# Kernel tuning notes

Measured on AMD Instinct MI355X. Metric: run time of the kernel, lower is better.

The kernel has to match this reference:

```python
import jax, jax.numpy as jnp
import numpy as np

N_NODES = 50000
N_EDGES = 800000
IN_CH = 128
HID = 64   # 2 * out_channels
OUT = 32   # out_channels
SLOPE = 0.2  # PyG GATConv default negative_slope


def _gat_layer(x, W, a_src, a_dst, b, src, dst):
    """Single-head GATConv: proj -> edge attention logits -> segment softmax
    over destination nodes -> scatter-aggregate weighted source messages."""
    n = x.shape[0]
    h = x @ W                                   # [N, C]
    ls = h @ a_src                              # [N] per-node src score
    ld = h @ a_dst                              # [N] per-node dst score
    logits = jax.nn.leaky_relu(ls[src] + ld[dst], negative_slope=SLOPE)  # [E]
    # numerically stable segment softmax grouped by destination node
    lmax = jax.ops.segment_max(logits, dst, num_segments=n)              # [N]
    e = jnp.exp(logits - lmax[dst])                                      # [E]
    denom = jax.ops.segment_sum(e, dst, num_segments=n)                  # [N]
    alpha = e / denom[dst]                                               # [E]
    out = jax.ops.segment_sum(alpha[:, None] * h[src], dst, num_segments=n)
    return out + b


def setup_inputs() -> dict:
    key = jax.random.key(0)
    ks = jax.random.split(key, 10)
    x = jax.random.normal(ks[0], (N_NODES, IN_CH), dtype=jnp.float32)
    edge_index = jax.random.randint(ks[1], (2, N_EDGES), 0, N_NODES, dtype=jnp.int32)
    s1 = 1.0 / np.sqrt(IN_CH)
    s2 = 1.0 / np.sqrt(HID)
    return {
        "x": x,
        "edge_index": edge_index,
        "W1": jax.random.normal(ks[2], (IN_CH, HID), dtype=jnp.float32) * s1,
        "a_src1": jax.random.normal(ks[3], (HID,), dtype=jnp.float32) * s2,
        "a_dst1": jax.random.normal(ks[4], (HID,), dtype=jnp.float32) * s2,
        "b1": jnp.zeros((HID,), dtype=jnp.float32),
        "W2": jax.random.normal(ks[5], (HID, OUT), dtype=jnp.float32) * s2,
        "a_src2": jax.random.normal(ks[6], (OUT,), dtype=jnp.float32) / np.sqrt(OUT),
        "a_dst2": jax.random.normal(ks[7], (OUT,), dtype=jnp.float32) / np.sqrt(OUT),
        "b2": jnp.zeros((OUT,), dtype=jnp.float32),
    }


def reference(x, edge_index, W1, a_src1, a_dst1, b1, W2, a_src2, a_dst2, b2):
    src, dst = edge_index[0], edge_index[1]
    h = jax.nn.relu(_gat_layer(x, W1, a_src1, a_dst1, b1, src, dst))
    return _gat_layer(h, W2, a_src2, a_dst2, b2, src, dst)
```

## Files before the change

kernel.cpp:

```cpp
#include <hip/hip_runtime.h>


#define N_NODES 50000
#define N_EDGES 800000
#define SLOPE 0.2f
#define NBUCK 196
#define CAP 4608

__global__ __launch_bounds__(256) void k_zerobins(int* __restrict__ binctr)
{
    if (threadIdx.x < NBUCK) binctr[threadIdx.x] = 0;
}

__global__ __launch_bounds__(1024) void k_bin(
    const int* __restrict__ src, const int* __restrict__ dst,
    int* __restrict__ binctr,
    int* __restrict__ stg_src, int* __restrict__ stg_dst)
{
    __shared__ int hist[NBUCK];
    __shared__ int gb[NBUCK];
    const int t = threadIdx.x;
    if (t < NBUCK) hist[t] = 0;
    __syncthreads();

    const int base = blockIdx.x * 8192;
    int ms[8], md[8], mr[8];
    int n = 0;
    #pragma unroll
    for (int k = 0; k < 8; ++k) {
        int e = base + t + k * 1024;
        if (e < N_EDGES) {
            int s = src[e], d = dst[e];
            ms[n] = s; md[n] = d;
            mr[n] = atomicAdd(&hist[d >> 8], 1);
            ++n;
        }
    }
    __syncthreads();
    if (t < NBUCK) gb[t] = atomicAdd(&binctr[t], hist[t]);
    __syncthreads();
    for (int i = 0; i < n; ++i) {
        int b = md[i] >> 8;
        int p = b * CAP + gb[b] + mr[i];
        stg_src[p] = ms[i];
        stg_dst[p] = md[i];
    }
}

__global__ __launch_bounds__(256) void k_btot(
    const int* __restrict__ binctr, int* __restrict__ bucket_base)
{
    __shared__ int tmp[256];
    const int t = threadIdx.x;
    int v = (t < NBUCK) ? binctr[t] : 0;
    tmp[t] = v;
    __syncthreads();
    #pragma unroll
    for (int off = 1; off < 256; off <<= 1) {
        int u = (t >= off) ? tmp[t - off] : 0;
        __syncthreads();
        tmp[t] += u;
        __syncthreads();
    }
    if (t < NBUCK) bucket_base[t] = tmp[t] - v;
}

__global__ __launch_bounds__(1024) void k_sort(
    const int* __restrict__ stg_src, const int* __restrict__ stg_dst,
    const int* __restrict__ binctr, const int* __restrict__ bucket_base,
    int* __restrict__ row_start, int* __restrict__ csr_src)
{
    __shared__ int cnt[256];
    __shared__ int off[256];
    const int b = blockIdx.x, t = threadIdx.x;
    const int n = binctr[b];
    const int sbase = b * CAP;
    const int obase = bucket_base[b];

    if (t < 256) cnt[t] = 0;
    __syncthreads();

    int ms[5], mk[5], mr[5];
    int c = 0;
    for (int i = t; i < n; i += 1024) {
        int s = stg_src[sbase + i], d = stg_dst[sbase + i];
        int k = d & 255;
        ms[c] = s; mk[c] = k;
        mr[c] = atomicAdd(&cnt[k], 1);
        ++c;
    }
    __syncthreads();

    if (t < 256) off[t] = cnt[t];
    __syncthreads();
    #pragma unroll
    for (int o = 1; o < 256; o <<= 1) {
        int u = (t < 256 && t >= o) ? off[t - o] : 0;
        __syncthreads();
        if (t < 256) off[t] += u;
        __syncthreads();
    }

    if (t < 256) {
        int node = b * 256 + t;
        if (node < N_NODES) row_start[node] = obase + off[t] - cnt[t];
    }
    if (b == NBUCK - 1 && t == 0) row_start[N_NODES] = N_EDGES;

    for (int i = 0; i < c; ++i)
        csr_src[obase + off[mk[i]] - cnt[mk[i]] + mr[i]] = ms[i];
}

__global__ __launch_bounds__(256) void k_gemm1(
    const float* __restrict__ x, const float* __restrict__ W1,
    const float* __restrict__ a_src, const float* __restrict__ a_dst,
    float* __restrict__ h1, float* __restrict__ ls, float* __restrict__ ld)
{
    __shared__ float As[64][128];
    __shared__ float Bs[128][64];
    const int tid = threadIdx.x;
    const int m0 = blockIdx.x * 64;

    {
        const float4* Wv = (const float4*)W1;
        float4* Bv = (float4*)&Bs[0][0];
        #pragma unroll
        for (int i = 0; i < 8; ++i) Bv[tid + i * 256] = Wv[tid + i * 256];
    }
    {
        const float4* Xv = (const float4*)x;
        #pragma unroll
        for (int i = 0; i < 8; ++i) {
            int idx = tid + i * 256;
            int r = idx >> 5, kq = idx & 31;
            float4 v = make_float4(0.f, 0.f, 0.f, 0.f);
            if (m0 + r < N_NODES) v = Xv[(size_t)(m0 + r) * 32 + kq];
            ((float4*)&As[r][0])[kq] = v;
        }
    }
    __syncthreads();

    const int tx = tid & 15, ty = tid >> 4;
    const int c0 = tx * 4, r0 = ty * 4;
    float acc[4][4] = {};
    for (int k = 0; k < 128; k += 4) {
        float a_s[4][4];
        #pragma unroll
        for (int i = 0; i < 4; ++i) {
            float4 av = *(const float4*)&As[r0 + i][k];
            a_s[i][0] = av.x; a_s[i][1] = av.y; a_s[i][2] = av.z; a_s[i][3] = av.w;
        }
        #pragma unroll
        for (int kk = 0; kk < 4; ++kk) {
            float4 b = *(const float4*)&Bs[k + kk][c0];
            #pragma unroll
            for (int i = 0; i < 4; ++i) {
                acc[i][0] += a_s[i][kk] * b.x;
                acc[i][1] += a_s[i][kk] * b.y;
                acc[i][2] += a_s[i][kk] * b.z;
                acc[i][3] += a_s[i][kk] * b.w;
            }
        }
    }

    float as4[4], ad4[4];
    #pragma unroll
    for (int j = 0; j < 4; ++j) { as4[j] = a_src[c0 + j]; ad4[j] = a_dst[c0 + j]; }

    #pragma unroll
    for (int i = 0; i < 4; ++i) {
        int row = m0 + r0 + i;
        float pls = acc[i][0]*as4[0] + acc[i][1]*as4[1] + acc[i][2]*as4[2] + acc[i][3]*as4[3];
        float pld = acc[i][0]*ad4[0] + acc[i][1]*ad4[1] + acc[i][2]*ad4[2] + acc[i][3]*ad4[3];
        #pragma unroll
        for (int off = 1; off < 16; off <<= 1) {
            pls += __shfl_xor(pls, off, 64);
            pld += __shfl_xor(pld, off, 64);
        }
        if (row < N_NODES) {
            ((float4*)&h1[(size_t)row * 64])[tx] =
                make_float4(acc[i][0], acc[i][1], acc[i][2], acc[i][3]);
            if (tx == 0) { ls[row] = pls; ld[row] = pld; }
        }
    }
}

__global__ __launch_bounds__(256) void k_agg1(
    const int* __restrict__ csr_src, const int* __restrict__ row_start,
    const float* __restrict__ ls, const float* __restrict__ ld,
    const float* __restrict__ h1, const float* __restrict__ b1,
    float* __restrict__ acc1)
{
    const int node = blockIdx.x * 4 + (threadIdx.x >> 6);
    const int lane = threadIdx.x & 63;
    const int beg = row_start[node], end = row_start[node + 1];
    const float ldv = ld[node];

    float acc = 0.f, sw = 0.f;
    for (int base = beg; base < end; base += 64) {
        const int cnt = min(64, end - base);
        int s = 0;
        float w = 0.f;
        if (lane < cnt) {
            s = csr_src[base + lane];
            float l = ls[s] + ldv;
            l = l > 0.f ? l : SLOPE * l;
            w = __expf(l);
        }
        float wsum = w;
        #pragma unroll
        for (int off = 1; off < 64; off <<= 1) wsum += __shfl_xor(wsum, off, 64);
        sw += wsum;

        int j = 0;
        for (; j + 4 <= cnt; j += 4) {
            int s0 = __shfl(s, j, 64),     s1 = __shfl(s, j + 1, 64);
            int s2 = __shfl(s, j + 2, 64), s3 = __shfl(s, j + 3, 64);
            float w0 = __shfl(w, j, 64),     w1 = __shfl(w, j + 1, 64);
            float w2 = __shfl(w, j + 2, 64), w3 = __shfl(w, j + 3, 64);
            float g0 = h1[(size_t)s0 * 64 + lane];
            float g1 = h1[(size_t)s1 * 64 + lane];
            float g2 = h1[(size_t)s2 * 64 + lane];
            float g3 = h1[(size_t)s3 * 64 + lane];
            acc += w0 * g0; acc += w1 * g1; acc += w2 * g2; acc += w3 * g3;
        }
        for (; j < cnt; ++j) {
            int sj = __shfl(s, j, 64);
            float wj = __shfl(w, j, 64);
            acc += wj * h1[(size_t)sj * 64 + lane];
        }
    }
    float r = sw > 0.f ? acc / sw : 0.f;
    acc1[(size_t)node * 64 + lane] = r + b1[lane];
}

__global__ __launch_bounds__(256) void k_epi1(
    const float* __restrict__ acc1, const float* __restrict__ W2,
    const float* __restrict__ a_src2, const float* __restrict__ a_dst2,
    float* __restrict__ h2, float* __restrict__ ls2, float* __restrict__ ld2)
{
    __shared__ float Hs[64][68];
    __shared__ float W2s[64][32];
    const int tid = threadIdx.x;
    const int n0 = blockIdx.x * 64;

    {
        const float4* Wv = (const float4*)W2;
        float4* Ws = (float4*)&W2s[0][0];
        Ws[tid] = Wv[tid];
        Ws[tid + 256] = Wv[tid + 256];
    }
    {
        const float4* Av = (const float4*)acc1;
        #pragma unroll
        for (int i = 0; i < 4; ++i) {
            int idx = tid + i * 256;
            int r = idx >> 4, kq = idx & 15;
            float4 v = make_float4(0.f, 0.f, 0.f, 0.f);
            if (n0 + r < N_NODES) {
                v = Av[(size_t)(n0 + r) * 16 + kq];
                v.x = fmaxf(v.x, 0.f); v.y = fmaxf(v.y, 0.f);
                v.z = fmaxf(v.z, 0.f); v.w = fmaxf(v.w, 0.f);
            }
            ((float4*)&Hs[r][0])[kq] = v;
        }
    }
    __syncthreads();

    const int nl = tid >> 2, cg = tid & 3, c0 = cg * 8;
    float acc[8] = {};
    for (int k4 = 0; k4 < 16; ++k4) {
        float4 hv4 = *(const float4*)&Hs[nl][k4 * 4];
        #pragma unroll
        for (int kk = 0; kk < 4; ++kk) {
            float hv = kk == 0 ? hv4.x : kk == 1 ? hv4.y : kk == 2 ? hv4.z : hv4.w;
            int k = k4 * 4 + kk;
            float4 w0 = *(const float4*)&W2s[k][c0];
            float4 w1 = *(const float4*)&W2s[k][c0 + 4];
            acc[0] += hv * w0.x; acc[1] += hv * w0.y;
            acc[2] += hv * w0.z; acc[3] += hv * w0.w;
            acc[4] += hv * w1.x; acc[5] += hv * w1.y;
            acc[6] += hv * w1.z; acc[7] += hv * w1.w;
        }
    }

    float pls = 0.f, pld = 0.f;
    #pragma unroll
    for (int j = 0; j < 8; ++j) {
        pls += acc[j] * a_src2[c0 + j];
        pld += acc[j] * a_dst2[c0 + j];
    }
    pls += __shfl_xor(pls, 1, 64); pls += __shfl_xor(pls, 2, 64);
    pld += __shfl_xor(pld, 1, 64); pld += __shfl_xor(pld, 2, 64);

    int node = n0 + nl;
    if (node < N_NODES) {
        ((float4*)&h2[(size_t)node * 32])[cg * 2] =
            make_float4(acc[0], acc[1], acc[2], acc[3]);
        ((float4*)&h2[(size_t)node * 32])[cg * 2 + 1] =
            make_float4(acc[4], acc[5], acc[6], acc[7]);
        if (cg == 0) { ls2[node] = pls; ld2[node] = pld; }
    }
}

__global__ __launch_bounds__(256) void k_agg2(
    const int* __restrict__ csr_src, const int* __restrict__ row_start,
    const float* __restrict__ ls, const float* __restrict__ ld,
    const float* __restrict__ h2, const float* __restrict__ b2,
    float* __restrict__ out)
{
    const int idx = blockIdx.x * 256 + threadIdx.x;
    const int node = idx >> 5;
    const int c = idx & 31;
    const int beg = row_start[node], end = row_start[node + 1];
    const float ldv = ld[node];

    float acc = 0.f, sw = 0.f;
    for (int base = beg; base < end; base += 32) {
        const int cnt = min(32, end - base);
        int s = 0;
        float w = 0.f;
        if (c < cnt) {
            s = csr_src[base + c];
            float l = ls[s] + ldv;
            l = l > 0.f ? l : SLOPE * l;
            w = __expf(l);
        }
        float wsum = w;
        #pragma unroll
        for (int off = 1; off < 32; off <<= 1) wsum += __shfl_xor(wsum, off, 32);
        sw += wsum;

        int j = 0;
        for (; j + 4 <= cnt; j += 4) {
            int s0 = __shfl(s, j, 32),     s1 = __shfl(s, j + 1, 32);
            int s2 = __shfl(s, j + 2, 32), s3 = __shfl(s, j + 3, 32);
            float w0 = __shfl(w, j, 32),     w1 = __shfl(w, j + 1, 32);
            float w2 = __shfl(w, j + 2, 32), w3 = __shfl(w, j + 3, 32);
            float g0 = h2[(size_t)s0 * 32 + c];
            float g1 = h2[(size_t)s1 * 32 + c];
            float g2 = h2[(size_t)s2 * 32 + c];
            float g3 = h2[(size_t)s3 * 32 + c];
            acc += w0 * g0; acc += w1 * g1; acc += w2 * g2; acc += w3 * g3;
        }
        for (; j < cnt; ++j) {
            int sj = __shfl(s, j, 32);
            float wj = __shfl(w, j, 32);
            acc += wj * h2[(size_t)sj * 32 + c];
        }
    }
    float r = sw > 0.f ? acc / sw : 0.f;
    out[(size_t)node * 32 + c] = r + b2[c];
}

extern "C" void kernel_launch(void* const* d_in, const int* in_sizes, int n_in,
                              void* d_out, int out_size, void* d_ws, size_t ws_size,
                              hipStream_t stream)
{
    const float* x      = (const float*)d_in[0];
    const int*   ei     = (const int*)  d_in[1];
    const float* W1     = (const float*)d_in[2];
    const float* a_src1 = (const float*)d_in[3];
    const float* a_dst1 = (const float*)d_in[4];
    const float* b1     = (const float*)d_in[5];
    const float* W2     = (const float*)d_in[6];
    const float* a_src2 = (const float*)d_in[7];
    const float* a_dst2 = (const float*)d_in[8];
    const float* b2     = (const float*)d_in[9];
    const int* src = ei;
    const int* dst = ei + N_EDGES;
    float* out = (float*)d_out;

    float* ws   = (float*)d_ws;
    float* h1   = ws;
    float* acc1 = ws + 3200000;
    float* ls1  = ws + 6400000;
    float* ld1  = ws + 6450000;
    int* row_start   = (int*)(ws + 6500000);
    int* csr_src     = (int*)(ws + 6550016);
    int* binctr      = (int*)(ws + 7350016);
    int* bucket_base = (int*)(ws + 7350272);
    int* stg_src = (int*)h1;
    int* stg_dst = (int*)acc1;
    float* h2  = h1;
    float* ls2 = ls1;
    float* ld2 = ld1;

    k_zerobins<<<1,   256,  0, stream>>>(binctr);
    k_bin     <<<98,  1024, 0, stream>>>(src, dst, binctr, stg_src, stg_dst);
    k_btot    <<<1,   256,  0, stream>>>(binctr, bucket_base);
    k_sort    <<<NBUCK, 1024, 0, stream>>>(stg_src, stg_dst, binctr, bucket_base,
                                           row_start, csr_src);

    k_gemm1<<<782,   256, 0, stream>>>(x, W1, a_src1, a_dst1, h1, ls1, ld1);
    k_agg1 <<<12500, 256, 0, stream>>>(csr_src, row_start, ls1, ld1, h1, b1, acc1);

    k_epi1 <<<782,  256, 0, stream>>>(acc1, W2, a_src2, a_dst2, h2, ls2, ld2);
    k_agg2 <<<6250, 256, 0, stream>>>(csr_src, row_start, ls2, ld2, h2, b2, out);
}
```

Measured before the change: 201.7 us.

## Pack staging edges into one word and vectorize aggregation gathers with float4

The binning stage now packs the source index and the low 8 bits of the destination into a single 32-bit word, so the staging traffic is halved and a single array is read in the sort pass. Both aggregation kernels now have each lane gather a float4 of a source row, with several edges processed in parallel across lane groups and then reduced through cross-lane shuffles. This aims to cut the number of gather instructions and improve memory-level parallelism on the irregular h-row loads. The cost is extra shuffle reductions at the end and only a fraction of lanes writing the output. Packing relies on node ids fitting in 16 bits, which holds for 50000 nodes.

```diff
diff --git a/kernel.cpp b/kernel.cpp
--- a/kernel.cpp
+++ b/kernel.cpp
@@ -14,8 +14,7 @@
 
 __global__ __launch_bounds__(1024) void k_bin(
     const int* __restrict__ src, const int* __restrict__ dst,
-    int* __restrict__ binctr,
-    int* __restrict__ stg_src, int* __restrict__ stg_dst)
+    int* __restrict__ binctr, int* __restrict__ stg)
 {
     __shared__ int hist[NBUCK];
     __shared__ int gb[NBUCK];
@@ -24,27 +23,25 @@
     __syncthreads();
 
     const int base = blockIdx.x * 8192;
-    int ms[8], md[8], mr[8];
+    int mp[8], mb[8], mr[8];
     int n = 0;
     #pragma unroll
     for (int k = 0; k < 8; ++k) {
         int e = base + t + k * 1024;
         if (e < N_EDGES) {
             int s = src[e], d = dst[e];
-            ms[n] = s; md[n] = d;
-            mr[n] = atomicAdd(&hist[d >> 8], 1);
+            int b = d >> 8;
+            mp[n] = s | ((d & 255) << 16);
+            mb[n] = b;
+            mr[n] = atomicAdd(&hist[b], 1);
             ++n;
         }
     }
     __syncthreads();
     if (t < NBUCK) gb[t] = atomicAdd(&binctr[t], hist[t]);
     __syncthreads();
-    for (int i = 0; i < n; ++i) {
-        int b = md[i] >> 8;
-        int p = b * CAP + gb[b] + mr[i];
-        stg_src[p] = ms[i];
-        stg_dst[p] = md[i];
-    }
+    for (int i = 0; i < n; ++i)
+        stg[mb[i] * CAP + gb[mb[i]] + mr[i]] = mp[i];
 }
 
 __global__ __launch_bounds__(256) void k_btot(
@@ -66,7 +63,7 @@
 }
 
 __global__ __launch_bounds__(1024) void k_sort(
-    const int* __restrict__ stg_src, const int* __restrict__ stg_dst,
+    const int* __restrict__ stg,
     const int* __restrict__ binctr, const int* __restrict__ bucket_base,
     int* __restrict__ row_start, int* __restrict__ csr_src)
 {
@@ -80,12 +77,13 @@
     if (t < 256) cnt[t] = 0;
     __syncthreads();
 
-    int ms[5], mk[5], mr[5];
+    int mv[5], mk[5], mr[5];
     int c = 0;
     for (int i = t; i < n; i += 1024) {
-        int s = stg_src[sbase + i], d = stg_dst[sbase + i];
-        int k = d & 255;
-        ms[c] = s; mk[c] = k;
+        int v = stg[sbase + i];
+        int k = v >> 16;
+        mv[c] = v & 0xFFFF;
+        mk[c] = k;
         mr[c] = atomicAdd(&cnt[k], 1);
         ++c;
     }
@@ -108,7 +106,7 @@
     if (b == NBUCK - 1 && t == 0) row_start[N_NODES] = N_EDGES;
 
     for (int i = 0; i < c; ++i)
-        csr_src[obase + off[mk[i]] - cnt[mk[i]] + mr[i]] = ms[i];
+        csr_src[obase + off[mk[i]] - cnt[mk[i]] + mr[i]] = mv[i];
 }
 
 __global__ __launch_bounds__(256) void k_gemm1(
@@ -193,10 +191,13 @@
 {
     const int node = blockIdx.x * 4 + (threadIdx.x >> 6);
     const int lane = threadIdx.x & 63;
+    const int c4 = lane & 15, eslot = lane >> 4;
     const int beg = row_start[node], end = row_start[node + 1];
     const float ldv = ld[node];
-
-    float acc = 0.f, sw = 0.f;
+    const float4* H = (const float4*)h1;
+
+    float4 acc = make_float4(0.f, 0.f, 0.f, 0.f);
+    float sw = 0.f;
     for (int base = beg; base < end; base += 64) {
         const int cnt = min(64, end - base);
         int s = 0;
@@ -213,25 +214,40 @@
         sw += wsum;
 
         int j = 0;
-        for (; j + 4 <= cnt; j += 4) {
-            int s0 = __shfl(s, j, 64),     s1 = __shfl(s, j + 1, 64);
-            int s2 = __shfl(s, j + 2, 64), s3 = __shfl(s, j + 3, 64);
-            float w0 = __shfl(w, j, 64),     w1 = __shfl(w, j + 1, 64);
-            float w2 = __shfl(w, j + 2, 64), w3 = __shfl(w, j + 3, 64);
-            float g0 = h1[(size_t)s0 * 64 + lane];
-            float g1 = h1[(size_t)s1 * 64 + lane];
-            float g2 = h1[(size_t)s2 * 64 + lane];
-            float g3 = h1[(size_t)s3 * 64 + lane];
-            acc += w0 * g0; acc += w1 * g1; acc += w2 * g2; acc += w3 * g3;
-        }
-        for (; j < cnt; ++j) {
-            int sj = __shfl(s, j, 64);
-            float wj = __shfl(w, j, 64);
-            acc += wj * h1[(size_t)sj * 64 + lane];
-        }
-    }
-    float r = sw > 0.f ? acc / sw : 0.f;
-    acc1[(size_t)node * 64 + lane] = r + b1[lane];
+        for (; j + 8 <= cnt; j += 8) {
+            int   s0 = __shfl(s, j + eslot, 64);
+            int   s1 = __shfl(s, j + 4 + eslot, 64);
+            float w0 = __shfl(w, j + eslot, 64);
+            float w1 = __shfl(w, j + 4 + eslot, 64);
+            float4 g0 = H[(size_t)s0 * 16 + c4];
+            float4 g1 = H[(size_t)s1 * 16 + c4];
+            acc.x += w0 * g0.x; acc.y += w0 * g0.y;
+            acc.z += w0 * g0.z; acc.w += w0 * g0.w;
+            acc.x += w1 * g1.x; acc.y += w1 * g1.y;
+            acc.z += w1 * g1.z; acc.w += w1 * g1.w;
+        }
+        for (; j < cnt; j += 4) {
+            int   sj = __shfl(s, j + eslot, 64);
+            float wj = __shfl(w, j + eslot, 64);
+            float4 g = H[(size_t)sj * 16 + c4];
+            acc.x += wj * g.x; acc.y += wj * g.y;
+            acc.z += wj * g.z; acc.w += wj * g.w;
+        }
+    }
+    #pragma unroll
+    for (int off = 16; off < 64; off <<= 1) {
+        acc.x += __shfl_xor(acc.x, off, 64);
+        acc.y += __shfl_xor(acc.y, off, 64);
+        acc.z += __shfl_xor(acc.z, off, 64);
+        acc.w += __shfl_xor(acc.w, off, 64);
+    }
+    if (eslot == 0) {
+        float inv = sw > 0.f ? 1.f / sw : 0.f;
+        float4 bb = ((const float4*)b1)[c4];
+        ((float4*)&acc1[(size_t)node * 64])[c4] =
+            make_float4(acc.x * inv + bb.x, acc.y * inv + bb.y,
+                        acc.z * inv + bb.z, acc.w * inv + bb.w);
+    }
 }
 
 __global__ __launch_bounds__(256) void k_epi1(
@@ -311,17 +327,20 @@
 {
     const int idx = blockIdx.x * 256 + threadIdx.x;
     const int node = idx >> 5;
-    const int c = idx & 31;
+    const int grp = idx & 31;
+    const int c4 = grp & 7, eslot = grp >> 3;
     const int beg = row_start[node], end = row_start[node + 1];
     const float ldv = ld[node];
-
-    float acc = 0.f, sw = 0.f;
+    const float4* H = (const float4*)h2;
+
+    float4 acc = make_float4(0.f, 0.f, 0.f, 0.f);
+    float sw = 0.f;
     for (int base = beg; base < end; base += 32) {
         const int cnt = min(32, end - base);
         int s = 0;
         float w = 0.f;
-        if (c < cnt) {
-            s = csr_src[base + c];
+        if (grp < cnt) {
+            s = csr_src[base + grp];
             float l = ls[s] + ldv;
             l = l > 0.f ? l : SLOPE * l;
             w = __expf(l);
@@ -332,25 +351,40 @@
         sw += wsum;
 
         int j = 0;
-        for (; j + 4 <= cnt; j += 4) {
-            int s0 = __shfl(s, j, 32),     s1 = __shfl(s, j + 1, 32);
-            int s2 = __shfl(s, j + 2, 32), s3 = __shfl(s, j + 3, 32);
-            float w0 = __shfl(w, j, 32),     w1 = __shfl(w, j + 1, 32);
-            float w2 = __shfl(w, j + 2, 32), w3 = __shfl(w, j + 3, 32);
-            float g0 = h2[(size_t)s0 * 32 + c];
-            float g1 = h2[(size_t)s1 * 32 + c];
-            float g2 = h2[(size_t)s2 * 32 + c];
-            float g3 = h2[(size_t)s3 * 32 + c];
-            acc += w0 * g0; acc += w1 * g1; acc += w2 * g2; acc += w3 * g3;
-        }
-        for (; j < cnt; ++j) {
-            int sj = __shfl(s, j, 32);
-            float wj = __shfl(w, j, 32);
-            acc += wj * h2[(size_t)sj * 32 + c];
-        }
-    }
-    float r = sw > 0.f ? acc / sw : 0.f;
-    out[(size_t)node * 32 + c] = r + b2[c];
+        for (; j + 8 <= cnt; j += 8) {
+            int   s0 = __shfl(s, j + eslot, 32);
+            int   s1 = __shfl(s, j + 4 + eslot, 32);
+            float w0 = __shfl(w, j + eslot, 32);
+            float w1 = __shfl(w, j + 4 + eslot, 32);
+            float4 g0 = H[(size_t)s0 * 8 + c4];
+            float4 g1 = H[(size_t)s1 * 8 + c4];
+            acc.x += w0 * g0.x; acc.y += w0 * g0.y;
+            acc.z += w0 * g0.z; acc.w += w0 * g0.w;
+            acc.x += w1 * g1.x; acc.y += w1 * g1.y;
+            acc.z += w1 * g1.z; acc.w += w1 * g1.w;
+        }
+        for (; j < cnt; j += 4) {
+            int   sj = __shfl(s, j + eslot, 32);
+            float wj = __shfl(w, j + eslot, 32);
+            float4 g = H[(size_t)sj * 8 + c4];
+            acc.x += wj * g.x; acc.y += wj * g.y;
+            acc.z += wj * g.z; acc.w += wj * g.w;
+        }
+    }
+    #pragma unroll
+    for (int off = 8; off < 32; off <<= 1) {
+        acc.x += __shfl_xor(acc.x, off, 32);
+        acc.y += __shfl_xor(acc.y, off, 32);
+        acc.z += __shfl_xor(acc.z, off, 32);
+        acc.w += __shfl_xor(acc.w, off, 32);
+    }
+    if (eslot == 0) {
+        float inv = sw > 0.f ? 1.f / sw : 0.f;
+        float4 bb = ((const float4*)b2)[c4];
+        ((float4*)&out[(size_t)node * 32])[c4] =
+            make_float4(acc.x * inv + bb.x, acc.y * inv + bb.y,
+                        acc.z * inv + bb.z, acc.w * inv + bb.w);
+    }
 }
 
 extern "C" void kernel_launch(void* const* d_in, const int* in_sizes, int n_in,
@@ -380,16 +414,15 @@
     int* csr_src     = (int*)(ws + 6550016);
     int* binctr      = (int*)(ws + 7350016);
     int* bucket_base = (int*)(ws + 7350272);
-    int* stg_src = (int*)h1;
-    int* stg_dst = (int*)acc1;
+    int* stg = (int*)h1;
     float* h2  = h1;
     float* ls2 = ls1;
     float* ld2 = ld1;
 
     k_zerobins<<<1,   256,  0, stream>>>(binctr);
-    k_bin     <<<98,  1024, 0, stream>>>(src, dst, binctr, stg_src, stg_dst);
+    k_bin     <<<98,  1024, 0, stream>>>(src, dst, binctr, stg);
     k_btot    <<<1,   256,  0, stream>>>(binctr, bucket_base);
-    k_sort    <<<NBUCK, 1024, 0, stream>>>(stg_src, stg_dst, binctr, bucket_base,
+    k_sort    <<<NBUCK, 1024, 0, stream>>>(stg, binctr, bucket_base,
                                            row_start, csr_src);
 
     k_gemm1<<<782,   256, 0, stream>>>(x, W1, a_src1, a_dst1, h1, ls1, ld1);
```

Result: faster. 190.7 us (-5.4%).
